# Kernel tuning notes

Measured on AMD Instinct MI355X. Metric: run time of the kernel, lower is better.

The kernel has to match this reference:

```python
import jax, jax.numpy as jnp
import numpy as np

NUM_HEADS = 12
N_SAMPLE = 60
COS_LOW = 0.7
COS_HIGH = 0.9
EPS = 1e-12  # F.normalize eps


def _l2norm(x, axis=-1):
    n = jnp.linalg.norm(x, axis=axis, keepdims=True)
    return x / jnp.maximum(n, EPS)


def get_random_attn(rng, v, n_sample, cos_low, cos_high):
    # v: (B, S) -- the CLS attention-score row per batch-head
    norm = jnp.linalg.norm(v, axis=-1, keepdims=True)            # (B, 1)
    u = _l2norm(v)                                               # (B, S)
    u = jnp.broadcast_to(u[None], (n_sample,) + v.shape)         # (n, B, S)
    k1, k2 = jax.random.split(rng)
    r = jax.random.uniform(k1, u.shape, dtype=v.dtype) * 2 - 1   # (n, B, S)
    a = jnp.einsum('nbd,nbd->nb', r, u)[..., None]               # (n, B, 1)
    uperp = _l2norm(r - a * u)                                   # (n, B, S)
    cos = (jax.random.uniform(k2, (n_sample,), dtype=v.dtype)
           * (cos_high - cos_low) + cos_low)[:, None, None]      # (n, 1, 1)
    w = cos * u + jnp.sqrt(1 - cos ** 2) * uperp                 # (n, B, S)
    return jnp.transpose(w * norm[None], (1, 0, 2))              # (B, n, S)


def setup_inputs() -> dict:
    key = jax.random.key(0)
    ks = jax.random.split(key, 8)
    L, N, E = 197, 128, 768
    s = 0.02
    return {
        'query': jax.random.normal(ks[0], (L, N, E), jnp.float32),
        'key': jax.random.normal(ks[1], (L, N, E), jnp.float32),
        'value': jax.random.normal(ks[2], (L, N, E), jnp.float32),
        'in_proj_weight': jax.random.normal(ks[3], (3 * E, E), jnp.float32) * s,
        'in_proj_bias': jax.random.normal(ks[4], (3 * E,), jnp.float32) * s,
        'out_proj_weight': jax.random.normal(ks[5], (E, E), jnp.float32) * s,
        'out_proj_bias': jax.random.normal(ks[6], (E,), jnp.float32) * s,
    }


def reference(query, key, value, in_proj_weight, in_proj_bias,
              out_proj_weight, out_proj_bias):
    L, N, E = query.shape
    H = NUM_HEADS
    hd = E // H
    # packed in-projection (separate q/k/v tensors -> chunked weights)
    w_q, w_k, w_v = jnp.split(in_proj_weight, 3, axis=0)
    b_q, b_k, b_v = jnp.split(in_proj_bias, 3, axis=0)
    q = query @ w_q.T + b_q
    k = key @ w_k.T + b_k
    v = value @ w_v.T + b_v
    # (L, N, E) -> (N*H, L, hd)
    q = jnp.transpose(q.reshape(L, N * H, hd), (1, 0, 2))
    k = jnp.transpose(k.reshape(L, N * H, hd), (1, 0, 2))
    v = jnp.transpose(v.reshape(L, N * H, hd), (1, 0, 2))
    q = q / jnp.sqrt(jnp.asarray(hd, q.dtype))
    attn = jnp.einsum('bte,bse->bts', q, k)                      # (B, L, S)
    center = attn[:, 0, :]                                        # (B, S)
    rand_rows = get_random_attn(jax.random.key(1234), center,
                                N_SAMPLE, COS_LOW, COS_HIGH)      # (B, n, S)
    attn = jnp.concatenate([attn[:, :1, :], rand_rows, attn[:, 1:, :]], axis=1)
    attn = jax.nn.softmax(attn, axis=-1)                          # (B, L+n, S)
    out = jnp.einsum('bts,bse->bte', attn, v)                     # (B, L+n, hd)
    Lt = L + N_SAMPLE
    out = jnp.transpose(out, (1, 0, 2)).reshape(Lt, N, E)
    out = out @ out_proj_weight.T + out_proj_bias                 # (Lt, N, E)
    attn_weights = attn.reshape(N, H, Lt, L).mean(axis=1)         # averaged heads
    return out, attn_weights
```

## Files before the change

### kernel.cpp

```cpp
#include <hip/hip_runtime.h>
#include <stdint.h>

constexpr int Lc  = 197;
constexpr int Nc  = 128;
constexpr int Ec  = 768;
constexpr int HDc = 64;
constexpr int Bc  = Nc * 12;
constexpr int LTc = Lc + 60;
constexpr float EPSc = 1e-12f;

struct U2 { uint32_t x, y; };

__device__ __forceinline__ U2 tf2x32(uint32_t k0, uint32_t k1, uint32_t x0, uint32_t x1) {
  uint32_t k2 = k0 ^ k1 ^ 0x1BD11BDAu;
  x0 += k0; x1 += k1;
#define TFR(r) { x0 += x1; x1 = (x1 << (r)) | (x1 >> (32 - (r))); x1 ^= x0; }
  TFR(13) TFR(15) TFR(26) TFR(6)
  x0 += k1; x1 += k2 + 1u;
  TFR(17) TFR(29) TFR(16) TFR(24)
  x0 += k2; x1 += k0 + 2u;
  TFR(13) TFR(15) TFR(26) TFR(6)
  x0 += k0; x1 += k1 + 3u;
  TFR(17) TFR(29) TFR(16) TFR(24)
  x0 += k1; x1 += k2 + 4u;
  TFR(13) TFR(15) TFR(26) TFR(6)
  x0 += k2; x1 += k0 + 5u;
#undef TFR
  return {x0, x1};
}

__device__ __forceinline__ float u01f(uint32_t bits) {
  return __uint_as_float((bits >> 9) | 0x3f800000u) - 1.0f;
}

__device__ __forceinline__ uint32_t rbits(uint32_t ka, uint32_t kb, uint32_t idx) {
  U2 r = tf2x32(ka, kb, 0u, idx);
  return r.x ^ r.y;
}

__device__ __forceinline__ void split_keys(uint32_t& k1a, uint32_t& k1b, uint32_t& k2a, uint32_t& k2b) {
  U2 t0 = tf2x32(0u, 1234u, 0u, 0u); k1a = t0.x; k1b = t0.y;
  U2 t1 = tf2x32(0u, 1234u, 0u, 1u); k2a = t1.x; k2b = t1.y;
}

__device__ __forceinline__ float rdlane(float v, int l) {
  return __int_as_float(__builtin_amdgcn_readlane(__float_as_int(v), l));
}

__device__ __forceinline__ void f2hilo(float f, unsigned short& h, unsigned short& l) {
  uint32_t u = __float_as_uint(f);
  h = (unsigned short)(u >> 16);
  float lof = f - __uint_as_float(u & 0xffff0000u);
  l = (unsigned short)(__float_as_uint(lof) >> 16);
}

__device__ __forceinline__ unsigned short bf16rne(float f) {
  uint32_t u = __float_as_uint(f);
  u += 0x7fffu + ((u >> 16) & 1u);
  return (unsigned short)(u >> 16);
}

__global__ __launch_bounds__(256) void convert_hilo(const float* __restrict__ src,
                                                    unsigned short* __restrict__ dst,
                                                    int rows)
{
  int idx = blockIdx.x * 256 + threadIdx.x;
  int total = rows * 192;
  if (idx >= total) return;
  int m = idx / 192, c = (idx % 192) * 4;
  float4 f = *(const float4*)(src + (size_t)m * 768 + c);
  ushort4 hv, lv;
  f2hilo(f.x, hv.x, lv.x);
  f2hilo(f.y, hv.y, lv.y);
  f2hilo(f.z, hv.z, lv.z);
  f2hilo(f.w, hv.w, lv.w);
  *(ushort4*)(dst + (size_t)m * 1536 + c) = hv;
  *(ushort4*)(dst + (size_t)m * 1536 + 768 + c) = lv;
}

typedef __attribute__((ext_vector_type(8))) short bfrag_t;
typedef __attribute__((ext_vector_type(4))) float accfrag_t;

template <int MODE>
__global__ __launch_bounds__(256) void gemm_mfma(
    const unsigned short* __restrict__ A0, const unsigned short* __restrict__ A1,
    const unsigned short* __restrict__ A2in, const unsigned short* __restrict__ Wb,
    const float* __restrict__ bias, int cb,
    float* __restrict__ O0, float* __restrict__ O1, float* __restrict__ O2)
{
  __shared__ unsigned short As[128 * 40];
  __shared__ unsigned short Bs[128 * 40];
  const int bm = blockIdx.x;
  const int bn = cb + blockIdx.y;
  const int tid = threadIdx.x;
  const int lane = tid & 63, wv = tid >> 6;
  const int wm = (wv & 1) * 64, wn = (wv >> 1) * 64;
  const int q4 = lane >> 4, l16 = lane & 15;

  const unsigned short* A;
  int which = 0;
  if (MODE == 0) { which = bn / 6; A = which == 0 ? A0 : (which == 1 ? A1 : A2in); }
  else A = A0;

  const int sr = tid >> 2;
  const int sc = (tid & 3) * 8;

  accfrag_t acc[4][4];
#pragma unroll
  for (int i = 0; i < 4; i++)
#pragma unroll
    for (int j = 0; j < 4; j++)
#pragma unroll
      for (int r = 0; r < 4; r++) acc[i][j][r] = 0.0f;

  for (int kt = 0; kt < 48; kt++) {
    const int k0 = kt * 32;
    __syncthreads();
#pragma unroll
    for (int p = 0; p < 2; p++) {
      int r = p * 64 + sr;
      uint4 av = *(const uint4*)(A  + (size_t)(bm * 128 + r) * 1536 + k0 + sc);
      *(uint4*)&As[r * 40 + sc] = av;
      uint4 bv = *(const uint4*)(Wb + (size_t)(bn * 128 + r) * 1536 + k0 + sc);
      *(uint4*)&Bs[r * 40 + sc] = bv;
    }
    __syncthreads();
    bfrag_t af[4], bf[4];
#pragma unroll
    for (int i = 0; i < 4; i++) {
      af[i] = *(const bfrag_t*)&As[(wm + i * 16 + l16) * 40 + q4 * 8];
      bf[i] = *(const bfrag_t*)&Bs[(wn + i * 16 + l16) * 40 + q4 * 8];
    }
#pragma unroll
    for (int i = 0; i < 4; i++)
#pragma unroll
      for (int j = 0; j < 4; j++)
        acc[i][j] = __builtin_amdgcn_mfma_f32_16x16x32_bf16(af[i], bf[j], acc[i][j], 0, 0, 0);
  }

  float bv4[4];
#pragma unroll
  for (int j = 0; j < 4; j++) bv4[j] = bias[bn * 128 + wn + j * 16 + l16];

  if (MODE == 0) {
    const float scale = (which == 0) ? 0.125f : 1.0f;
    float* O = which == 0 ? O0 : (which == 1 ? O1 : O2);
#pragma unroll
    for (int i = 0; i < 4; i++) {
#pragma unroll
      for (int r = 0; r < 4; r++) {
        int m = bm * 128 + wm + i * 16 + q4 * 4 + r;
        int l = m >> 7, nb = m & 127;
#pragma unroll
        for (int j = 0; j < 4; j++) {
          int ng = bn * 128 + wn + j * 16 + l16;
          int nc = ng - which * 768;
          int h = nc >> 6, d = nc & 63;
          O[(((size_t)(nb * 12 + h)) * 197 + l) * 64 + d] = (acc[i][j][r] + bv4[j]) * scale;
        }
      }
    }
  } else {
#pragma unroll
    for (int i = 0; i < 4; i++) {
#pragma unroll
      for (int r = 0; r < 4; r++) {
        int m = bm * 128 + wm + i * 16 + q4 * 4 + r;
#pragma unroll
        for (int j = 0; j < 4; j++) {
          int ng = bn * 128 + wn + j * 16 + l16;
          O0[(size_t)m * 768 + ng] = acc[i][j][r] + bv4[j];
        }
      }
    }
  }
}

__global__ __launch_bounds__(256) void center_kernel(
    const float* __restrict__ q_ws, const float* __restrict__ k_ws,
    float* __restrict__ center, float* __restrict__ cnorm)
{
  const int b = blockIdx.x;
  const int lane = threadIdx.x & 63, w = threadIdx.x >> 6;
  __shared__ float ssh[4];
  const float q0 = q_ws[(size_t)b * (197 * 64) + lane];
  float ss = 0.0f;
  for (int s = w; s < 197; s += 4) {
    float val = q0 * k_ws[((size_t)b * 197 + s) * 64 + lane];
#pragma unroll
    for (int off = 32; off >= 1; off >>= 1) val += __shfl_xor(val, off, 64);
    if (lane == 0) center[(size_t)b * 197 + s] = val;
    ss += val * val;
  }
  if (lane == 0) ssh[w] = ss;
  __syncthreads();
  if (threadIdx.x == 0) cnorm[b] = sqrtf(ssh[0] + ssh[1] + ssh[2] + ssh[3]);
}

__device__ __forceinline__ void softmax4(float x[4][4], bool v3, float p[4][4])
{
  float m[4], s[4];
#pragma unroll
  for (int i = 0; i < 4; i++) {
    m[i] = fmaxf(fmaxf(x[i][0], x[i][1]), x[i][2]);
    if (v3) m[i] = fmaxf(m[i], x[i][3]);
  }
#pragma unroll
  for (int off = 32; off >= 1; off >>= 1) {
#pragma unroll
    for (int i = 0; i < 4; i++) m[i] = fmaxf(m[i], __shfl_xor(m[i], off, 64));
  }
#pragma unroll
  for (int i = 0; i < 4; i++) {
    float e0 = __expf(x[i][0] - m[i]);
    float e1 = __expf(x[i][1] - m[i]);
    float e2 = __expf(x[i][2] - m[i]);
    float e3 = v3 ? __expf(x[i][3] - m[i]) : 0.0f;
    p[i][0] = e0; p[i][1] = e1; p[i][2] = e2; p[i][3] = e3;
    s[i] = e0 + e1 + e2 + e3;
  }
#pragma unroll
  for (int off = 32; off >= 1; off >>= 1) {
#pragma unroll
    for (int i = 0; i < 4; i++) s[i] += __shfl_xor(s[i], off, 64);
  }
#pragma unroll
  for (int i = 0; i < 4; i++) {
    float rs = 1.0f / s[i];
    p[i][0] *= rs; p[i][1] *= rs; p[i][2] *= rs; p[i][3] *= rs;
  }
}

__device__ __forceinline__ void weights_add(float* __restrict__ awn, int t, int lane,
                                            bool v3, const float* p)
{
  float* a = awn + (size_t)t * 197;
  const float c = 1.0f / 12.0f;
  atomicAdd(a + lane, p[0] * c);
  atomicAdd(a + lane + 64, p[1] * c);
  atomicAdd(a + lane + 128, p[2] * c);
  if (v3) atomicAdd(a + lane + 192, p[3] * c);
}

__global__ __launch_bounds__(512, 2) void attn_kernel(
    const float* __restrict__ q_ws, const float* __restrict__ k_ws, const float* __restrict__ v_ws,
    const float* __restrict__ center, const float* __restrict__ cnorm,
    unsigned short* __restrict__ A2, float* __restrict__ attn_w)
{
  __shared__ float kT[64][201];
  __shared__ __align__(16) unsigned short Vth[64 * 232];
  __shared__ __align__(16) unsigned short Vtl[64 * 232];
  __shared__ __align__(16) unsigned short Pl[32 * 232];
  __shared__ float cen[200];
  __shared__ float uu[200];

  const int b = blockIdx.x;
  const int n = b / 12, h = b % 12;
  const int tid = threadIdx.x;
  const int lane = tid & 63, w = tid >> 6;
  const int q4 = lane >> 4, l16 = lane & 15;
  const bool v3 = lane < 5;

  const float* kg = k_ws + (size_t)b * (197 * 64);
  const float* vg = v_ws + (size_t)b * (197 * 64);
  const float* qg = q_ws + (size_t)b * (197 * 64);

  for (int idx = tid; idx < 64 * 35; idx += 512) {
    int d = idx / 35, s = 197 + idx % 35;
    Vth[d * 232 + s] = 0;
    Vtl[d * 232 + s] = 0;
  }
  for (int idx = tid; idx < 32 * 35; idx += 512) {
    int r = idx / 35, s = 197 + idx % 35;
    Pl[r * 232 + s] = 0;
  }

  for (int idx = tid; idx < 197 * 64; idx += 512) {
    int s = idx >> 6, d = idx & 63;
    kT[d][s] = kg[idx];
    unsigned short vh, vl;
    f2hilo(vg[idx], vh, vl);
    Vth[d * 232 + s] = vh;
    Vtl[d * 232 + s] = vl;
  }
  {
    float inv = 1.0f / fmaxf(cnorm[b], EPSc);
    for (int s = tid; s < 197; s += 512) {
      float c = center[(size_t)b * 197 + s];
      cen[s] = c;
      uu[s] = c * inv;
    }
  }
  __syncthreads();

  const float us0 = uu[lane], us1 = uu[lane + 64], us2 = uu[lane + 128];
  const float us3 = v3 ? uu[lane + 192] : 0.0f;

  const float cnb = cnorm[b];
  uint32_t k1a, k1b, k2a, k2b;
  split_keys(k1a, k1b, k2a, k2b);
  float* awn = attn_w + (size_t)n * (LTc * 197);

  for (int c = 0; c < 9; c++) {
    const int t0 = c * 32 + w * 4;
    const bool sact = (c < 8) || (w == 0);

    if (sact) {
      float x[4][4];
      if (t0 + 3 >= 61) {
        float qr[4];
#pragma unroll
        for (int i = 0; i < 4; i++) {
          int l = t0 + i - 60;
          l = l < 0 ? 0 : (l > 196 ? 196 : l);
          qr[i] = qg[(size_t)l * 64 + lane];
        }
#pragma unroll
        for (int i = 0; i < 4; i++)
#pragma unroll
          for (int j = 0; j < 4; j++) x[i][j] = 0.0f;
#pragma unroll 4
        for (int d = 0; d < 64; d++) {
          float q0 = rdlane(qr[0], d), q1 = rdlane(qr[1], d);
          float q2 = rdlane(qr[2], d), q3 = rdlane(qr[3], d);
          float kv0 = kT[d][lane], kv1 = kT[d][lane + 64], kv2 = kT[d][lane + 128];
          float kv3 = v3 ? kT[d][lane + 192] : 0.0f;
          x[0][0] = fmaf(q0, kv0, x[0][0]); x[0][1] = fmaf(q0, kv1, x[0][1]);
          x[0][2] = fmaf(q0, kv2, x[0][2]); x[0][3] = fmaf(q0, kv3, x[0][3]);
          x[1][0] = fmaf(q1, kv0, x[1][0]); x[1][1] = fmaf(q1, kv1, x[1][1]);
          x[1][2] = fmaf(q1, kv2, x[1][2]); x[1][3] = fmaf(q1, kv3, x[1][3]);
          x[2][0] = fmaf(q2, kv0, x[2][0]); x[2][1] = fmaf(q2, kv1, x[2][1]);
          x[2][2] = fmaf(q2, kv2, x[2][2]); x[2][3] = fmaf(q2, kv3, x[2][3]);
          x[3][0] = fmaf(q3, kv0, x[3][0]); x[3][1] = fmaf(q3, kv1, x[3][1]);
          x[3][2] = fmaf(q3, kv2, x[3][2]); x[3][3] = fmaf(q3, kv3, x[3][3]);
        }
      }
#pragma unroll
      for (int i = 0; i < 4; i++) {
        const int t = t0 + i;
        if (t >= 61) continue;
        if (t == 0) {
          x[0][0] = cen[lane]; x[0][1] = cen[lane + 64]; x[0][2] = cen[lane + 128];
          x[0][3] = v3 ? cen[lane + 192] : 0.0f;
        } else {
          const int ns = t - 1;
          const uint32_t base = ((uint32_t)ns * 1536u + (uint32_t)b) * 197u;
          float r0 = u01f(rbits(k1a, k1b, base + lane))       * 2.0f - 1.0f;
          float r1 = u01f(rbits(k1a, k1b, base + lane + 64))  * 2.0f - 1.0f;
          float r2 = u01f(rbits(k1a, k1b, base + lane + 128)) * 2.0f - 1.0f;
          float r3 = v3 ? (u01f(rbits(k1a, k1b, base + lane + 192)) * 2.0f - 1.0f) : 0.0f;
          float pa = r0 * us0 + r1 * us1 + r2 * us2 + r3 * us3;
#pragma unroll
          for (int off = 32; off >= 1; off >>= 1) pa += __shfl_xor(pa, off, 64);
          float rp0 = r0 - pa * us0, rp1 = r1 - pa * us1;
          float rp2 = r2 - pa * us2, rp3 = r3 - pa * us3;
          float sq2 = rp0 * rp0 + rp1 * rp1 + rp2 * rp2 + (v3 ? rp3 * rp3 : 0.0f);
#pragma unroll
          for (int off = 32; off >= 1; off >>= 1) sq2 += __shfl_xor(sq2, off, 64);
          float invn = 1.0f / fmaxf(sqrtf(sq2), EPSc);
          float cv = u01f(rbits(k2a, k2b, (uint32_t)ns)) * 0.2f + 0.7f;
          float sv = sqrtf(1.0f - cv * cv);
          float f = sv * invn;
          x[i][0] = cnb * (cv * us0 + f * rp0);
          x[i][1] = cnb * (cv * us1 + f * rp1);
          x[i][2] = cnb * (cv * us2 + f * rp2);
          x[i][3] = cnb * (cv * us3 + f * rp3);
        }
      }
      float pr[4][4];
      softmax4(x, v3, pr);
#pragma unroll
      for (int i = 0; i < 4; i++)
        if (c < 8 || i == 0) weights_add(awn, t0 + i, lane, v3, pr[i]);
#pragma unroll
      for (int i = 0; i < 4; i++) {
        unsigned short* pRow = Pl + (w * 4 + i) * 232;
        pRow[lane]       = bf16rne(pr[i][0]);
        pRow[lane + 64]  = bf16rne(pr[i][1]);
        pRow[lane + 128] = bf16rne(pr[i][2]);
        if (v3) pRow[lane + 192] = bf16rne(pr[i][3]);
      }
    }
    __syncthreads();

    const bool pvact = (c < 8) || (w < 4);
    if (pvact) {
      const int tt = (c < 8) ? (w >> 2) : 0;
      const int dj = (c < 8) ? (w & 3) : w;
      accfrag_t acc = {0.0f, 0.0f, 0.0f, 0.0f};
      const unsigned short* pA = Pl  + (tt * 16 + l16) * 232 + q4 * 8;
      const unsigned short* pH = Vth + (dj * 16 + l16) * 232 + q4 * 8;
      const unsigned short* pL = Vtl + (dj * 16 + l16) * 232 + q4 * 8;
#pragma unroll
      for (int ks = 0; ks < 7; ks++) {
        bfrag_t af = *(const bfrag_t*)(pA + ks * 32);
        bfrag_t bh = *(const bfrag_t*)(pH + ks * 32);
        bfrag_t bl = *(const bfrag_t*)(pL + ks * 32);
        acc = __builtin_amdgcn_mfma_f32_16x16x32_bf16(af, bh, acc, 0, 0, 0);
        acc = __builtin_amdgcn_mfma_f32_16x16x32_bf16(af, bl, acc, 0, 0, 0);
      }
      const int tbase = c * 32 + tt * 16 + q4 * 4;
      const int d = dj * 16 + l16;
#pragma unroll
      for (int r = 0; r < 4; r++) {
        const int t = tbase + r;
        if (t <= 256) {
          unsigned short hb, lb;
          f2hilo(acc[r], hb, lb);
          size_t base = ((size_t)t * 128 + n) * 1536 + h * 64 + d;
          A2[base] = hb;
          A2[base + 768] = lb;
        }
      }
    }
    __syncthreads();
  }
}

extern "C" void kernel_launch(void* const* d_in, const int* in_sizes, int n_in,
                              void* d_out, int out_size, void* d_ws, size_t ws_size,
                              hipStream_t stream)
{
  const float* query = (const float*)d_in[0];
  const float* key   = (const float*)d_in[1];
  const float* value = (const float*)d_in[2];
  const float* w_in  = (const float*)d_in[3];
  const float* b_in  = (const float*)d_in[4];
  const float* w_out = (const float*)d_in[5];
  const float* b_out = (const float*)d_in[6];

  float* out    = (float*)d_out;
  float* attn_w = out + (size_t)LTc * Nc * Ec;

  constexpr size_t SZ_HEADF = (size_t)Bc * Lc * HDc * 4;
  constexpr size_t OFF_CEN  = 3 * SZ_HEADF;
  constexpr size_t OFF_CN   = OFF_CEN + (size_t)Bc * Lc * 4;
  constexpr size_t R0       = OFF_CN + 8192;
  constexpr size_t SZ_XB    = (size_t)25216 * 1536 * 2;
  constexpr size_t SZ_A2    = (size_t)LTc * Nc * 1536 * 2;
  constexpr size_t SZ_WB    = (size_t)2304 * 1536 * 2;
  constexpr size_t SZ_WOB   = (size_t)768 * 1536 * 2;
  constexpr size_t FULL_NEED = R0 + 3 * SZ_XB + SZ_WB + SZ_WOB;

  uint8_t* w8 = (uint8_t*)d_ws;
  float* q_ws   = (float*)w8;
  float* k_ws   = (float*)(w8 + SZ_HEADF);
  float* v_ws   = (float*)(w8 + 2 * SZ_HEADF);
  float* center = (float*)(w8 + OFF_CEN);
  float* cnorm  = (float*)(w8 + OFF_CN);
  unsigned short* A2b = (unsigned short*)(w8 + R0);

  const bool full = ws_size >= FULL_NEED;
  unsigned short* wb  = (unsigned short*)(w8 + (full ? (R0 + 3 * SZ_XB) : (R0 + SZ_XB)));
  unsigned short* wob = (unsigned short*)(w8 + (full ? (R0 + 3 * SZ_XB + SZ_WB) : (R0 + SZ_A2)));

  (void)in_sizes; (void)n_in; (void)out_size;

  convert_hilo<<<(2304 * 192 + 255) / 256, 256, 0, stream>>>(w_in, wb, 2304);
  convert_hilo<<<(768 * 192 + 255) / 256, 256, 0, stream>>>(w_out, wob, 768);

  const int xblk = (25216 * 192 + 255) / 256;
  if (full) {
    unsigned short* xb0 = (unsigned short*)(w8 + R0);
    unsigned short* xb1 = xb0 + SZ_XB / 2;
    unsigned short* xb2 = xb1 + SZ_XB / 2;
    convert_hilo<<<xblk, 256, 0, stream>>>(query, xb0, 25216);
    convert_hilo<<<xblk, 256, 0, stream>>>(key,   xb1, 25216);
    convert_hilo<<<xblk, 256, 0, stream>>>(value, xb2, 25216);
    gemm_mfma<0><<<dim3(197, 18), 256, 0, stream>>>(xb0, xb1, xb2, wb, b_in, 0,
                                                    q_ws, k_ws, v_ws);
  } else {
    unsigned short* buf = (unsigned short*)(w8 + R0);
    const float* xs[3] = {query, key, value};
    for (int wh = 0; wh < 3; wh++) {
      convert_hilo<<<xblk, 256, 0, stream>>>(xs[wh], buf, 25216);
      gemm_mfma<0><<<dim3(197, 6), 256, 0, stream>>>(buf, buf, buf, wb, b_in, 6 * wh,
                                                     q_ws, k_ws, v_ws);
    }
  }

  center_kernel<<<dim3(1536), 256, 0, stream>>>(q_ws, k_ws, center, cnorm);

  hipMemsetAsync(attn_w, 0, (size_t)Nc * LTc * Lc * sizeof(float), stream);

  attn_kernel<<<dim3(1536), 512, 0, stream>>>(q_ws, k_ws, v_ws, center, cnorm,
                                              A2b, attn_w);

  gemm_mfma<1><<<dim3(257, 6), 256, 0, stream>>>(A2b, nullptr, nullptr, wob, b_out, 0,
                                                 out, nullptr, nullptr);
}
```

Baseline: 1.428 ms.

## Use direct global-to-LDS loads in GEMM and double-buffer P in attention

The GEMM now stages A and W tiles with global_load_lds, which writes straight into LDS without passing through registers. To fit the contiguous layout that instruction requires, the LDS row padding (stride 40) is dropped for an unpadded stride of 32, which may add bank conflicts on the fragment reads. The attention kernel double-buffers the probability tile, so the softmax of chunk c overlaps the PV MFMA of chunk c-1 and one barrier per iteration is removed. This costs extra LDS for the second P buffer, which may lower occupancy.

Result: faster. 1.315 ms (-7.9%).

```diff
diff --git a/kernel.cpp b/kernel.cpp
--- a/kernel.cpp
+++ b/kernel.cpp
@@ -47,6 +47,11 @@
   return __int_as_float(__builtin_amdgcn_readlane(__float_as_int(v), l));
 }
 
+__device__ __forceinline__ void gl_lds16(const unsigned short* g, unsigned short* l) {
+  __builtin_amdgcn_global_load_lds((const __attribute__((address_space(1))) void*)g,
+                                   (__attribute__((address_space(3))) void*)l, 16, 0, 0);
+}
+
 __device__ __forceinline__ void f2hilo(float f, unsigned short& h, unsigned short& l) {
   uint32_t u = __float_as_uint(f);
   h = (unsigned short)(u >> 16);
@@ -88,8 +93,8 @@
     const float* __restrict__ bias, int cb,
     float* __restrict__ O0, float* __restrict__ O1, float* __restrict__ O2)
 {
-  __shared__ unsigned short As[128 * 40];
-  __shared__ unsigned short Bs[128 * 40];
+  __shared__ __align__(16) unsigned short As[128 * 32];
+  __shared__ __align__(16) unsigned short Bs[128 * 32];
   const int bm = blockIdx.x;
   const int bn = cb + blockIdx.y;
   const int tid = threadIdx.x;
@@ -102,8 +107,8 @@
   if (MODE == 0) { which = bn / 6; A = which == 0 ? A0 : (which == 1 ? A1 : A2in); }
   else A = A0;
 
-  const int sr = tid >> 2;
-  const int sc = (tid & 3) * 8;
+  const int srow = wv * 16 + (lane >> 2);
+  const int scol = (lane & 3) * 8;
 
   accfrag_t acc[4][4];
 #pragma unroll
@@ -116,20 +121,16 @@
   for (int kt = 0; kt < 48; kt++) {
     const int k0 = kt * 32;
     __syncthreads();
-#pragma unroll
-    for (int p = 0; p < 2; p++) {
-      int r = p * 64 + sr;
-      uint4 av = *(const uint4*)(A  + (size_t)(bm * 128 + r) * 1536 + k0 + sc);
-      *(uint4*)&As[r * 40 + sc] = av;
-      uint4 bv = *(const uint4*)(Wb + (size_t)(bn * 128 + r) * 1536 + k0 + sc);
-      *(uint4*)&Bs[r * 40 + sc] = bv;
-    }
+    gl_lds16(A  + (size_t)(bm * 128 + srow) * 1536 + k0 + scol,      &As[wv * 512]);
+    gl_lds16(Wb + (size_t)(bn * 128 + srow) * 1536 + k0 + scol,      &Bs[wv * 512]);
+    gl_lds16(A  + (size_t)(bm * 128 + 64 + srow) * 1536 + k0 + scol, &As[2048 + wv * 512]);
+    gl_lds16(Wb + (size_t)(bn * 128 + 64 + srow) * 1536 + k0 + scol, &Bs[2048 + wv * 512]);
     __syncthreads();
     bfrag_t af[4], bf[4];
 #pragma unroll
     for (int i = 0; i < 4; i++) {
-      af[i] = *(const bfrag_t*)&As[(wm + i * 16 + l16) * 40 + q4 * 8];
-      bf[i] = *(const bfrag_t*)&Bs[(wn + i * 16 + l16) * 40 + q4 * 8];
+      af[i] = *(const bfrag_t*)&As[(wm + i * 16 + l16) * 32 + q4 * 8];
+      bf[i] = *(const bfrag_t*)&Bs[(wn + i * 16 + l16) * 32 + q4 * 8];
     }
 #pragma unroll
     for (int i = 0; i < 4; i++)
@@ -250,7 +251,7 @@
   __shared__ float kT[64][201];
   __shared__ __align__(16) unsigned short Vth[64 * 232];
   __shared__ __align__(16) unsigned short Vtl[64 * 232];
-  __shared__ __align__(16) unsigned short Pl[32 * 232];
+  __shared__ __align__(16) unsigned short Pl[2][32 * 232];
   __shared__ float cen[200];
   __shared__ float uu[200];
 
@@ -270,9 +271,9 @@
     Vth[d * 232 + s] = 0;
     Vtl[d * 232 + s] = 0;
   }
-  for (int idx = tid; idx < 32 * 35; idx += 512) {
-    int r = idx / 35, s = 197 + idx % 35;
-    Pl[r * 232 + s] = 0;
+  for (int idx = tid; idx < 2 * 32 * 35; idx += 512) {
+    int bb = idx / (32 * 35), r = (idx / 35) & 31, s = 197 + idx % 35;
+    Pl[bb][r * 232 + s] = 0;
   }
 
   for (int idx = tid; idx < 197 * 64; idx += 512) {
@@ -301,119 +302,122 @@
   split_keys(k1a, k1b, k2a, k2b);
   float* awn = attn_w + (size_t)n * (LTc * 197);
 
-  for (int c = 0; c < 9; c++) {
-    const int t0 = c * 32 + w * 4;
-    const bool sact = (c < 8) || (w == 0);
-
-    if (sact) {
-      float x[4][4];
-      if (t0 + 3 >= 61) {
-        float qr[4];
+  for (int c = 0; c <= 9; c++) {
+    if (c <= 8) {
+      const int t0 = c * 32 + w * 4;
+      const bool sact = (c < 8) || (w == 0);
+      if (sact) {
+        float x[4][4];
+        if (t0 + 3 >= 61) {
+          float qr[4];
+#pragma unroll
+          for (int i = 0; i < 4; i++) {
+            int l = t0 + i - 60;
+            l = l < 0 ? 0 : (l > 196 ? 196 : l);
+            qr[i] = qg[(size_t)l * 64 + lane];
+          }
+#pragma unroll
+          for (int i = 0; i < 4; i++)
+#pragma unroll
+            for (int j = 0; j < 4; j++) x[i][j] = 0.0f;
+#pragma unroll 4
+          for (int d = 0; d < 64; d++) {
+            float q0 = rdlane(qr[0], d), q1 = rdlane(qr[1], d);
+            float q2 = rdlane(qr[2], d), q3 = rdlane(qr[3], d);
+            float kv0 = kT[d][lane], kv1 = kT[d][lane + 64], kv2 = kT[d][lane + 128];
+            float kv3 = v3 ? kT[d][lane + 192] : 0.0f;
+            x[0][0] = fmaf(q0, kv0, x[0][0]); x[0][1] = fmaf(q0, kv1, x[0][1]);
+            x[0][2] = fmaf(q0, kv2, x[0][2]); x[0][3] = fmaf(q0, kv3, x[0][3]);
+            x[1][0] = fmaf(q1, kv0, x[1][0]); x[1][1] = fmaf(q1, kv1, x[1][1]);
+            x[1][2] = fmaf(q1, kv2, x[1][2]); x[1][3] = fmaf(q1, kv3, x[1][3]);
+            x[2][0] = fmaf(q2, kv0, x[2][0]); x[2][1] = fmaf(q2, kv1, x[2][1]);
+            x[2][2] = fmaf(q2, kv2, x[2][2]); x[2][3] = fmaf(q2, kv3, x[2][3]);
+            x[3][0] = fmaf(q3, kv0, x[3][0]); x[3][1] = fmaf(q3, kv1, x[3][1]);
+            x[3][2] = fmaf(q3, kv2, x[3][2]); x[3][3] = fmaf(q3, kv3, x[3][3]);
+          }
+        }
 #pragma unroll
         for (int i = 0; i < 4; i++) {
-          int l = t0 + i - 60;
-          l = l < 0 ? 0 : (l > 196 ? 196 : l);
-          qr[i] = qg[(size_t)l * 64 + lane];
-        }
+          const int t = t0 + i;
+          if (t >= 61) continue;
+          if (t == 0) {
+            x[0][0] = cen[lane]; x[0][1] = cen[lane + 64]; x[0][2] = cen[lane + 128];
+            x[0][3] = v3 ? cen[lane + 192] : 0.0f;
+          } else {
+            const int ns = t - 1;
+            const uint32_t base = ((uint32_t)ns * 1536u + (uint32_t)b) * 197u;
+            float r0 = u01f(rbits(k1a, k1b, base + lane))       * 2.0f - 1.0f;
+            float r1 = u01f(rbits(k1a, k1b, base + lane + 64))  * 2.0f - 1.0f;
+            float r2 = u01f(rbits(k1a, k1b, base + lane + 128)) * 2.0f - 1.0f;
+            float r3 = v3 ? (u01f(rbits(k1a, k1b, base + lane + 192)) * 2.0f - 1.0f) : 0.0f;
+            float pa = r0 * us0 + r1 * us1 + r2 * us2 + r3 * us3;
+#pragma unroll
+            for (int off = 32; off >= 1; off >>= 1) pa += __shfl_xor(pa, off, 64);
+            float rp0 = r0 - pa * us0, rp1 = r1 - pa * us1;
+            float rp2 = r2 - pa * us2, rp3 = r3 - pa * us3;
+            float sq2 = rp0 * rp0 + rp1 * rp1 + rp2 * rp2 + (v3 ? rp3 * rp3 : 0.0f);
+#pragma unroll
+            for (int off = 32; off >= 1; off >>= 1) sq2 += __shfl_xor(sq2, off, 64);
+            float invn = 1.0f / fmaxf(sqrtf(sq2), EPSc);
+            float cv = u01f(rbits(k2a, k2b, (uint32_t)ns)) * 0.2f + 0.7f;
+            float sv = sqrtf(1.0f - cv * cv);
+            float f = sv * invn;
+            x[i][0] = cnb * (cv * us0 + f * rp0);
+            x[i][1] = cnb * (cv * us1 + f * rp1);
+            x[i][2] = cnb * (cv * us2 + f * rp2);
+            x[i][3] = cnb * (cv * us3 + f * rp3);
+          }
+        }
+        float pr[4][4];
+        softmax4(x, v3, pr);
 #pragma unroll
         for (int i = 0; i < 4; i++)
-#pragma unroll
-          for (int j = 0; j < 4; j++) x[i][j] = 0.0f;
-#pragma unroll 4
-        for (int d = 0; d < 64; d++) {
-          float q0 = rdlane(qr[0], d), q1 = rdlane(qr[1], d);
-          float q2 = rdlane(qr[2], d), q3 = rdlane(qr[3], d);
-          float kv0 = kT[d][lane], kv1 = kT[d][lane + 64], kv2 = kT[d][lane + 128];
-          float kv3 = v3 ? kT[d][lane + 192] : 0.0f;
-          x[0][0] = fmaf(q0, kv0, x[0][0]); x[0][1] = fmaf(q0, kv1, x[0][1]);
-          x[0][2] = fmaf(q0, kv2, x[0][2]); x[0][3] = fmaf(q0, kv3, x[0][3]);
-          x[1][0] = fmaf(q1, kv0, x[1][0]); x[1][1] = fmaf(q1, kv1, x[1][1]);
-          x[1][2] = fmaf(q1, kv2, x[1][2]); x[1][3] = fmaf(q1, kv3, x[1][3]);
-          x[2][0] = fmaf(q2, kv0, x[2][0]); x[2][1] = fmaf(q2, kv1, x[2][1]);
-          x[2][2] = fmaf(q2, kv2, x[2][2]); x[2][3] = fmaf(q2, kv3, x[2][3]);
-          x[3][0] = fmaf(q3, kv0, x[3][0]); x[3][1] = fmaf(q3, kv1, x[3][1]);
-          x[3][2] = fmaf(q3, kv2, x[3][2]); x[3][3] = fmaf(q3, kv3, x[3][3]);
+          if (c < 8 || i == 0) weights_add(awn, t0 + i, lane, v3, pr[i]);
+#pragma unroll
+        for (int i = 0; i < 4; i++) {
+          unsigned short* pRow = &Pl[c & 1][(w * 4 + i) * 232];
+          pRow[lane]       = bf16rne(pr[i][0]);
+          pRow[lane + 64]  = bf16rne(pr[i][1]);
+          pRow[lane + 128] = bf16rne(pr[i][2]);
+          if (v3) pRow[lane + 192] = bf16rne(pr[i][3]);
         }
       }
-#pragma unroll
-      for (int i = 0; i < 4; i++) {
-        const int t = t0 + i;
-        if (t >= 61) continue;
-        if (t == 0) {
-          x[0][0] = cen[lane]; x[0][1] = cen[lane + 64]; x[0][2] = cen[lane + 128];
-          x[0][3] = v3 ? cen[lane + 192] : 0.0f;
-        } else {
-          const int ns = t - 1;
-          const uint32_t base = ((uint32_t)ns * 1536u + (uint32_t)b) * 197u;
-          float r0 = u01f(rbits(k1a, k1b, base + lane))       * 2.0f - 1.0f;
-          float r1 = u01f(rbits(k1a, k1b, base + lane + 64))  * 2.0f - 1.0f;
-          float r2 = u01f(rbits(k1a, k1b, base + lane + 128)) * 2.0f - 1.0f;
-          float r3 = v3 ? (u01f(rbits(k1a, k1b, base + lane + 192)) * 2.0f - 1.0f) : 0.0f;
-          float pa = r0 * us0 + r1 * us1 + r2 * us2 + r3 * us3;
-#pragma unroll
-          for (int off = 32; off >= 1; off >>= 1) pa += __shfl_xor(pa, off, 64);
-          float rp0 = r0 - pa * us0, rp1 = r1 - pa * us1;
-          float rp2 = r2 - pa * us2, rp3 = r3 - pa * us3;
-          float sq2 = rp0 * rp0 + rp1 * rp1 + rp2 * rp2 + (v3 ? rp3 * rp3 : 0.0f);
-#pragma unroll
-          for (int off = 32; off >= 1; off >>= 1) sq2 += __shfl_xor(sq2, off, 64);
-          float invn = 1.0f / fmaxf(sqrtf(sq2), EPSc);
-          float cv = u01f(rbits(k2a, k2b, (uint32_t)ns)) * 0.2f + 0.7f;
-          float sv = sqrtf(1.0f - cv * cv);
-          float f = sv * invn;
-          x[i][0] = cnb * (cv * us0 + f * rp0);
-          x[i][1] = cnb * (cv * us1 + f * rp1);
-          x[i][2] = cnb * (cv * us2 + f * rp2);
-          x[i][3] = cnb * (cv * us3 + f * rp3);
+    }
+
+    if (c >= 1) {
+      const int cc = c - 1;
+      const bool pvact = (cc < 8) || (w < 4);
+      if (pvact) {
+        const int tt = (cc < 8) ? (w >> 2) : 0;
+        const int dj = (cc < 8) ? (w & 3) : w;
+        accfrag_t acc = {0.0f, 0.0f, 0.0f, 0.0f};
+        const unsigned short* pA = &Pl[cc & 1][(tt * 16 + l16) * 232] + q4 * 8;
+        const unsigned short* pH = Vth + (dj * 16 + l16) * 232 + q4 * 8;
+        const unsigned short* pL = Vtl + (dj * 16 + l16) * 232 + q4 * 8;
+#pragma unroll
+        for (int ks = 0; ks < 7; ks++) {
+          bfrag_t af = *(const bfrag_t*)(pA + ks * 32);
+          bfrag_t bh = *(const bfrag_t*)(pH + ks * 32);
+          bfrag_t bl = *(const bfrag_t*)(pL + ks * 32);
+          acc = __builtin_amdgcn_mfma_f32_16x16x32_bf16(af, bh, acc, 0, 0, 0);
+          acc = __builtin_amdgcn_mfma_f32_16x16x32_bf16(af, bl, acc, 0, 0, 0);
+        }
+        const int tbase = cc * 32 + tt * 16 + q4 * 4;
+        const int d = dj * 16 + l16;
+#pragma unroll
+        for (int r = 0; r < 4; r++) {
+          const int t = tbase + r;
+          if (t <= 256) {
+            unsigned short hb, lb;
+            f2hilo(acc[r], hb, lb);
+            size_t base = ((size_t)t * 128 + n) * 1536 + h * 64 + d;
+            A2[base] = hb;
+            A2[base + 768] = lb;
+          }
         }
       }
-      float pr[4][4];
-      softmax4(x, v3, pr);
-#pragma unroll
-      for (int i = 0; i < 4; i++)
-        if (c < 8 || i == 0) weights_add(awn, t0 + i, lane, v3, pr[i]);
-#pragma unroll
-      for (int i = 0; i < 4; i++) {
-        unsigned short* pRow = Pl + (w * 4 + i) * 232;
-        pRow[lane]       = bf16rne(pr[i][0]);
-        pRow[lane + 64]  = bf16rne(pr[i][1]);
-        pRow[lane + 128] = bf16rne(pr[i][2]);
-        if (v3) pRow[lane + 192] = bf16rne(pr[i][3]);
-      }
-    }
-    __syncthreads();
-
-    const bool pvact = (c < 8) || (w < 4);
-    if (pvact) {
-      const int tt = (c < 8) ? (w >> 2) : 0;
-      const int dj = (c < 8) ? (w & 3) : w;
-      accfrag_t acc = {0.0f, 0.0f, 0.0f, 0.0f};
-      const unsigned short* pA = Pl  + (tt * 16 + l16) * 232 + q4 * 8;
-      const unsigned short* pH = Vth + (dj * 16 + l16) * 232 + q4 * 8;
-      const unsigned short* pL = Vtl + (dj * 16 + l16) * 232 + q4 * 8;
-#pragma unroll
-      for (int ks = 0; ks < 7; ks++) {
-        bfrag_t af = *(const bfrag_t*)(pA + ks * 32);
-        bfrag_t bh = *(const bfrag_t*)(pH + ks * 32);
-        bfrag_t bl = *(const bfrag_t*)(pL + ks * 32);
-        acc = __builtin_amdgcn_mfma_f32_16x16x32_bf16(af, bh, acc, 0, 0, 0);
-        acc = __builtin_amdgcn_mfma_f32_16x16x32_bf16(af, bl, acc, 0, 0, 0);
-      }
-      const int tbase = c * 32 + tt * 16 + q4 * 4;
-      const int d = dj * 16 + l16;
-#pragma unroll
-      for (int r = 0; r < 4; r++) {
-        const int t = tbase + r;
-        if (t <= 256) {
-          unsigned short hb, lb;
-          f2hilo(acc[r], hb, lb);
-          size_t base = ((size_t)t * 128 + n) * 1536 + h * 64 + d;
-          A2[base] = hb;
-          A2[base + 768] = lb;
-        }
-      }
-    }
-    __syncthreads();
+    }
+    if (c < 9) __syncthreads();
   }
 }
 
```
